# Kernel optimization log

Measured on AMD Instinct MI355X. Metric: run time of the kernel, lower is better.

The kernel has to match this reference:

```python
import jax, jax.numpy as jnp
import numpy as np

B = 256          # graphs per batch
NN = 400         # ROI nodes per graph (N*(N-1)/2 = 79800 = input_dim)
HID = [32, 64, 128]
KS = [200, 100, 50]   # nodes kept after each TopKPooling (ratio 0.5 each)
EPS = 1e-5


def setup_inputs() -> dict:
    key = jax.random.key(0)
    ks = jax.random.split(key, 20)
    # flattened strict upper triangle of a nonnegative FC matrix per sample
    data = jax.random.uniform(ks[0], (B, NN * (NN - 1) // 2), dtype=jnp.float32)
    inp = {"data": data}
    dims = [1] + HID
    for l in range(3):
        fan_in = dims[l]
        inp[f"W{l+1}"] = jax.random.normal(ks[1 + 5 * l], (dims[l], dims[l + 1]), jnp.float32) / np.sqrt(fan_in)
        inp[f"b{l+1}"] = jnp.zeros((dims[l + 1],), jnp.float32)
        inp[f"g{l+1}"] = jnp.ones((dims[l + 1],), jnp.float32)      # BN gamma
        inp[f"be{l+1}"] = jnp.zeros((dims[l + 1],), jnp.float32)    # BN beta
        inp[f"p{l+1}"] = jax.random.normal(ks[4 + 5 * l], (dims[l + 1],), jnp.float32) * 0.1  # TopK score vector
    return inp


def _gcn_conv(A, X, W, b):
    # GCNConv with edge weights: add self loops (weight 1), symmetric D^-1/2 A D^-1/2
    n = A.shape[1]
    Al = A + jnp.eye(n, dtype=A.dtype)[None]          # (B, n, n)
    deg = Al.sum(axis=-1)                             # (B, n)
    dis = jnp.where(deg > 0, jax.lax.rsqrt(deg), 0.0)
    An = dis[:, :, None] * Al * dis[:, None, :]
    return jnp.einsum('bij,bjf->bif', An, X @ W) + b


def _block(A, X, W, b, g, be, p, k):
    # GCNConv -> ReLU -> BatchNorm(train stats) -> (dropout=identity) -> TopKPooling
    h = jax.nn.relu(_gcn_conv(A, X, W, b))
    mu = h.mean(axis=(0, 1))
    var = h.var(axis=(0, 1))
    h = (h - mu) * jax.lax.rsqrt(var + EPS) * g + be
    # TopKPooling: score = x . p / ||p||, keep top k per graph, gate by tanh(score)
    score = h @ p / jnp.linalg.norm(p)                # (B, n)
    vals, idx = jax.lax.top_k(score, k)               # (B, k)
    Xn = jnp.take_along_axis(h, idx[:, :, None], axis=1) * jnp.tanh(vals)[:, :, None]
    bi = jnp.arange(A.shape[0])[:, None, None]
    An = A[bi, idx[:, :, None], idx[:, None, :]]      # filter_adj: edges among kept nodes
    return An, Xn


def reference(data, W1, b1, g1, be1, p1, W2, b2, g2, be2, p2, W3, b3, g3, be3, p3):
    Bn = data.shape[0]
    iu0, iu1 = np.triu_indices(NN, 1)
    A = jnp.zeros((Bn, NN, NN), data.dtype).at[:, iu0, iu1].set(data)
    A = A + jnp.swapaxes(A, 1, 2)                     # symmetric FC adjacency, zero diag
    X = jnp.ones((Bn, NN, 1), data.dtype)             # initial node feature dim = 1
    A, X = _block(A, X, W1, b1, g1, be1, p1, KS[0])
    A, X = _block(A, X, W2, b2, g2, be2, p2, KS[1])
    A, X = _block(A, X, W3, b3, g3, be3, p3, KS[2])
    return X.max(axis=1)                              # global_max_pool -> (B, 128)
```

## Files before the change

### kernel.cpp

```cpp
#include <hip/hip_runtime.h>
#include <math.h>

#define BB   256
#define NN0  400
#define NE   79800
#define EPSF 1e-5f

__device__ __forceinline__ int tri_e(int a, int c) {
  return a*(NN0-1) - ((a*(a-1))>>1) + (c - a - 1);
}

__device__ __forceinline__ size_t PRI(int b, int ti, int tj, int r) {
  return (((size_t)b*7 + ti)*7 + tj)*64 + r;
}

__device__ __forceinline__ float wave_sum(float v) {
  #pragma unroll
  for (int o = 32; o > 0; o >>= 1) v += __shfl_xor(v, o, 64);
  return v;
}

__device__ __forceinline__ void bitonic_desc(float* sc, int* si, int P) {
  const int tid = threadIdx.x;
  for (int k = 2; k <= P; k <<= 1) {
    for (int j = k >> 1; j > 0; j >>= 1) {
      __syncthreads();
      for (int i = tid; i < P; i += 256) {
        int ixj = i ^ j;
        if (ixj > i) {
          float a = sc[i], c = sc[ixj];
          int ai = si[i], ci = si[ixj];
          bool bef = (a > c) || (a == c && ai < ci);
          bool sw = ((i & k) == 0) ? !bef : bef;
          if (sw) { sc[i] = c; sc[ixj] = a; si[i] = ci; si[ixj] = ai; }
        }
      }
    }
  }
  __syncthreads();
}

__global__ __launch_bounds__(256) void k_tri_mv(
    const float* __restrict__ data,
    const float* __restrict__ pr_in, const float* __restrict__ pc_in,
    float* __restrict__ pr, float* __restrict__ pc) {
  __shared__ float tile[64][65];
  __shared__ float dI[64], dJ[64];
  const int q0 = blockIdx.x % 7, b = blockIdx.x / 7;
  const int tid = threadIdx.x;
  const int wave = tid >> 6, lane = tid & 63;
  const float* __restrict__ drow = data + (size_t)b*NE;
  int ti_a[4], tj_a[4];
  #pragma unroll
  for (int u = 0; u < 4; ++u) {
    int t = q0 + u*7;
    int ti = 0, rem = t;
    while (rem >= 7 - ti) { rem -= 7 - ti; ++ti; }
    ti_a[u] = ti; tj_a[u] = ti + rem;
  }
  float vreg[16];
  float rI = 0.f, rJ = 0.f;
  auto issue = [&](int u) {
    const int i0 = ti_a[u]*64, j0 = tj_a[u]*64;
    const int ni = min(64, NN0 - i0), nj = min(64, NN0 - j0);
    #pragma unroll
    for (int k = 0; k < 16; ++k) {
      const int rr = wave*16 + k;
      const int i = i0 + rr, j = j0 + lane;
      vreg[k] = 0.f;
      if (rr < ni && lane < nj && j > i) vreg[k] = drow[tri_e(i, j)];
    }
    if (pr_in) {
      if (tid < 64) {
        float a = 0.f;
        if (tid < ni) {
          const int tt = ti_a[u], r = tid;
          float acc = 1.f;
          for (int tj = tt; tj < 7; ++tj) acc += pr_in[PRI(b, tt, tj, r)];
          for (int ts = 0; ts <= tt; ++ts) acc += pc_in[PRI(b, ts, tt, r)];
          a = rsqrtf(acc);
        }
        rI = a;
      } else if (tid < 128) {
        const int c = tid - 64;
        float a = 0.f;
        if (c < nj) {
          const int tt = tj_a[u], r = c;
          float acc = 1.f;
          for (int tj = tt; tj < 7; ++tj) acc += pr_in[PRI(b, tt, tj, r)];
          for (int ts = 0; ts <= tt; ++ts) acc += pc_in[PRI(b, ts, tt, r)];
          a = rsqrtf(acc);
        }
        rJ = a;
      }
    } else {
      if (tid < 64) rI = (tid < ni) ? 1.f : 0.f;
      else if (tid < 128) rJ = (tid - 64 < nj) ? 1.f : 0.f;
    }
  };
  issue(0);
  #pragma unroll 1
  for (int u = 0; u < 4; ++u) {
    const int ti = ti_a[u], tj = tj_a[u];
    if (u) __syncthreads();
    #pragma unroll
    for (int k = 0; k < 16; ++k) tile[wave*16 + k][lane] = vreg[k];
    if (tid < 64) dI[tid] = rI;
    else if (tid < 128) dJ[tid-64] = rJ;
    __syncthreads();
    if (u + 1 < 4) issue(u + 1);
    {
      const int r = tid >> 2, q = tid & 3;
      float s = 0.f;
      #pragma unroll
      for (int c = 0; c < 16; ++c) s += tile[r][q*16 + c] * dJ[q*16 + c];
      s += __shfl_xor(s, 1, 64);
      s += __shfl_xor(s, 2, 64);
      if (q == 0) pr[PRI(b, ti, tj, r)] = s;
    }
    {
      const int c = tid >> 2, q = tid & 3;
      float s = 0.f;
      #pragma unroll
      for (int r = 0; r < 16; ++r) s += tile[q*16 + r][c] * dI[q*16 + r];
      s += __shfl_xor(s, 1, 64);
      s += __shfl_xor(s, 2, 64);
      if (q == 0) pc[PRI(b, ti, tj, c)] = s;
    }
  }
}

__global__ __launch_bounds__(256) void k_sfin_stats_red(
    const float* __restrict__ pr, const float* __restrict__ pc,
    const float* __restrict__ pr2, const float* __restrict__ pc2,
    const float* __restrict__ W1, const float* __restrict__ b1,
    float* __restrict__ s1, float* __restrict__ acc1) {
  __shared__ float sl[256];
  __shared__ float st[64];
  __shared__ float w1s[32], b1s[32];
  const int tid = threadIdx.x;
  const int i = blockIdx.x*256 + tid;
  if (tid < 32) { w1s[tid] = W1[tid]; b1s[tid] = b1[tid]; }
  if (tid < 64) st[tid] = 0.f;
  const int b = i / NN0, n = i % NN0;
  const int t = n >> 6, r = n & 63;
  float dacc = 1.f, sacc = 0.f;
  for (int tj = t; tj < 7; ++tj) { dacc += pr[PRI(b, t, tj, r)]; sacc += pr2[PRI(b, t, tj, r)]; }
  for (int ti = 0; ti <= t; ++ti) { dacc += pc[PRI(b, ti, t, r)]; sacc += pc2[PRI(b, ti, t, r)]; }
  const float d = rsqrtf(dacc);
  const float s = d * (d + sacc);
  s1[i] = s;
  sl[tid] = s;
  __syncthreads();
  const int f = tid & 31, sub = tid >> 5;
  const float w = w1s[f], bb = b1s[f];
  float S = 0.f, Q = 0.f;
  #pragma unroll
  for (int k = 0; k < 32; ++k) {
    const float ss = sl[sub*32 + k];
    const float h = fmaxf(ss*w + bb, 0.f);
    S += h; Q += h*h;
  }
  atomicAdd(&st[f], S);
  atomicAdd(&st[32+f], Q);
  __syncthreads();
  if (tid < 64) atomicAdd(&acc1[tid], st[tid]);
}

__global__ __launch_bounds__(256) void k_top1(
    const float* __restrict__ s1, const float* __restrict__ acc1,
    const float* __restrict__ W1, const float* __restrict__ b1,
    const float* __restrict__ g1, const float* __restrict__ be1,
    const float* __restrict__ p1, const float* __restrict__ W2,
    int* __restrict__ nodes2, int* __restrict__ sperm2, float* __restrict__ Y2) {
  __shared__ float sc[512]; __shared__ int si[512];
  __shared__ float sS[NN0];
  __shared__ float tvs[200];
  __shared__ int nds_l[200];
  __shared__ float w1s[32], b1s[32], cfs[32], scs[32], shs[32];
  __shared__ __align__(16) float hp[6400];
  __shared__ float c0s;
  const int tid = threadIdx.x, b = blockIdx.x;
  if (tid < 32) { w1s[tid] = W1[tid]; b1s[tid] = b1[tid]; }
  if (tid < 64) {
    float scale = 0.f, shift = 0.f, pv = 0.f;
    if (tid < 32) {
      const float S = acc1[tid], Q = acc1[32 + tid];
      const float N = 102400.f;
      const float mu = S / N;
      const float var = Q / N - mu*mu;
      const float inv = rsqrtf(var + EPSF);
      scale = inv * g1[tid];
      shift = be1[tid] - mu * scale;
      pv = p1[tid];
    }
    const float pn = sqrtf(wave_sum(pv*pv));
    if (tid < 32) { scs[tid] = scale; shs[tid] = shift; cfs[tid] = scale*pv/pn; }
    float u = (tid < 32) ? shift*pv/pn : 0.f;
    u = wave_sum(u);
    if (tid == 0) c0s = u;
  }
  __syncthreads();
  const float c0 = c0s;
  for (int i = tid; i < 512; i += 256) {
    if (i < NN0) {
      const float s = s1[(size_t)b*NN0 + i];
      sS[i] = s;
      float sco = c0;
      #pragma unroll
      for (int f = 0; f < 32; ++f) sco += fmaxf(s*w1s[f] + b1s[f], 0.f) * cfs[f];
      sc[i] = sco; si[i] = i;
    } else { sc[i] = -INFINITY; si[i] = 0x7fffffff; }
  }
  bitonic_desc(sc, si, 512);
  for (int k = tid; k < 200; k += 256) {
    tvs[k] = tanhf(sc[k]);
    nds_l[k] = si[k];
    nodes2[b*200 + k] = si[k];
  }
  __syncthreads();
  for (int o = tid; o < 6400; o += 256) {
    const int k = o >> 5, f = o & 31;
    const float s = sS[nds_l[k]];
    const float h = fmaxf(s*w1s[f] + b1s[f], 0.f);
    hp[o] = (h*scs[f] + shs[f]) * tvs[k];
  }
  __syncthreads();
  {
    const int g = tid & 63;
    float wr[32];
    #pragma unroll
    for (int f = 0; f < 32; ++f) wr[f] = W2[f*64 + g];
    for (int o = tid; o < 12800; o += 256) {
      const int k = o >> 6;
      float acc = 0.f;
      #pragma unroll
      for (int c4 = 0; c4 < 8; ++c4) {
        const float4 x4 = *(const float4*)&hp[(k<<5) + (c4<<2)];
        acc += x4.x*wr[c4*4] + x4.y*wr[c4*4+1] + x4.z*wr[c4*4+2] + x4.w*wr[c4*4+3];
      }
      Y2[(size_t)b*12800 + o] = acc;
    }
  }
  __syncthreads();
  if (tid < 256) {
    sc[tid] = (tid < 200) ? -(float)nds_l[tid] : -INFINITY;
    si[tid] = (tid < 200) ? tid : 0x7fffffff;
  }
  bitonic_desc(sc, si, 256);
  if (tid < 200) sperm2[b*200 + tid] = si[tid];
}

__global__ __launch_bounds__(256) void k_gatherA2(
    const float* __restrict__ data, const int* __restrict__ nodes2,
    const int* __restrict__ sperm2, float* __restrict__ A2, float* __restrict__ dis2) {
  __shared__ int nds[200], sp[200], sn[200];
  __shared__ float rowbuf[4][200];
  const int idx = blockIdx.x;
  const int r9 = idx >> 3;
  const int b = (idx & 7)*32 + r9/50;
  const int rg = r9 % 50;
  const int tid = threadIdx.x;
  if (tid < 200) { nds[tid] = nodes2[b*200 + tid]; sp[tid] = sperm2[b*200 + tid]; }
  __syncthreads();
  if (tid < 200) sn[tid] = nds[sp[tid]];
  __syncthreads();
  const int wave = tid >> 6, lane = tid & 63;
  const int i = rg*4 + wave;
  const int ni = nds[i];
  const float* __restrict__ drow = data + (size_t)b*NE;
  float accd = 0.f;
  for (int jj = lane; jj < 200; jj += 64) {
    const int sj = sn[jj];
    float v = 0.f;
    if (sj != ni) {
      const int a = min(ni, sj), c = max(ni, sj);
      v = drow[tri_e(a, c)];
    }
    rowbuf[wave][sp[jj]] = v;
    accd += v;
  }
  __syncthreads();
  for (int j = lane; j < 200; j += 64)
    A2[((size_t)b*200 + i)*200 + j] = rowbuf[wave][j];
  accd = wave_sum(accd);
  if (lane == 0) dis2[b*200 + i] = rsqrtf(1.f + accd);
}

__global__ __launch_bounds__(256) void k_conv2(
    const float* __restrict__ A2, const float* __restrict__ Y2,
    const float* __restrict__ dis2, const float* __restrict__ b2,
    float* __restrict__ h2g, float* __restrict__ acc2g) {
  __shared__ __align__(16) float ab[40*64];
  __shared__ __align__(16) float zb[40*64];
  __shared__ float st[128];
  const int tid = threadIdx.x;
  const int b = blockIdx.x >> 2, p = blockIdx.x & 3;
  const int tx = tid & 15, ty = tid >> 4;
  if (tid < 128) st[tid] = 0.f;
  const float4 bv = *(const float4*)&b2[tx<<2];
  float acc[4][4] = {};
  #pragma unroll 1
  for (int j0 = 0; j0 < 200; j0 += 40) {
    __syncthreads();
    for (int t = tid; t < 640; t += 256) {
      const int js = t >> 4, f4 = t & 15;
      const float dz = dis2[b*200 + j0 + js];
      float4 v = *(const float4*)&Y2[((size_t)b*200 + (j0 + js))*64 + (f4 << 2)];
      v.x *= dz; v.y *= dz; v.z *= dz; v.w *= dz;
      *(float4*)&zb[(js << 6) + (f4 << 2)] = v;
    }
    for (int t = tid; t < 640; t += 256) {
      const int js = t >> 4, c4l = t & 15;
      const int cg = (p << 6) + (c4l << 2);
      float4 v = make_float4(0.f, 0.f, 0.f, 0.f);
      if (cg < 200)
        v = *(const float4*)&A2[((size_t)b*200 + (j0 + js))*200 + cg];
      *(float4*)&ab[(js << 6) + (c4l << 2)] = v;
    }
    __syncthreads();
    #pragma unroll 2
    for (int js = 0; js < 40; ++js) {
      const float4 a4 = *(const float4*)&ab[(js << 6) + (ty << 2)];
      const float4 z4 = *(const float4*)&zb[(js << 6) + (tx << 2)];
      acc[0][0] += a4.x*z4.x; acc[0][1] += a4.x*z4.y; acc[0][2] += a4.x*z4.z; acc[0][3] += a4.x*z4.w;
      acc[1][0] += a4.y*z4.x; acc[1][1] += a4.y*z4.y; acc[1][2] += a4.y*z4.z; acc[1][3] += a4.y*z4.w;
      acc[2][0] += a4.z*z4.x; acc[2][1] += a4.z*z4.y; acc[2][2] += a4.z*z4.z; acc[2][3] += a4.z*z4.w;
      acc[3][0] += a4.w*z4.x; acc[3][1] += a4.w*z4.y; acc[3][2] += a4.w*z4.z; acc[3][3] += a4.w*z4.w;
    }
  }
  float ss[4] = {0,0,0,0}, qq[4] = {0,0,0,0};
  #pragma unroll
  for (int qr = 0; qr < 4; ++qr) {
    const int r = (p << 6) + (ty << 2) + qr;
    if (r < 200) {
      const float d = dis2[b*200 + r];
      const float dd = d*d;
      const float4 zi = *(const float4*)&Y2[((size_t)b*200 + r)*64 + (tx << 2)];
      const float h0 = fmaxf(d*acc[qr][0] + dd*zi.x + bv.x, 0.f);
      const float h1 = fmaxf(d*acc[qr][1] + dd*zi.y + bv.y, 0.f);
      const float h2v = fmaxf(d*acc[qr][2] + dd*zi.z + bv.z, 0.f);
      const float h3v = fmaxf(d*acc[qr][3] + dd*zi.w + bv.w, 0.f);
      *(float4*)&h2g[((size_t)b*200 + r)*64 + (tx<<2)] = make_float4(h0,h1,h2v,h3v);
      ss[0]+=h0; ss[1]+=h1; ss[2]+=h2v; ss[3]+=h3v;
      qq[0]+=h0*h0; qq[1]+=h1*h1; qq[2]+=h2v*h2v; qq[3]+=h3v*h3v;
    }
  }
  #pragma unroll
  for (int qf = 0; qf < 4; ++qf) {
    atomicAdd(&st[(tx<<2)+qf], ss[qf]);
    atomicAdd(&st[64+(tx<<2)+qf], qq[qf]);
  }
  __syncthreads();
  if (tid < 128) atomicAdd(&acc2g[tid], st[tid]);
}

__global__ __launch_bounds__(256) void k_top2(
    const float* __restrict__ h2g, const float* __restrict__ acc2,
    const float* __restrict__ g2, const float* __restrict__ be2,
    const float* __restrict__ p2, const float* __restrict__ W3,
    const int* __restrict__ nodes2, int* __restrict__ nodes3,
    float* __restrict__ Y3) {
  __shared__ float sc[256]; __shared__ int si[256];
  __shared__ __align__(16) float xs[6400];
  __shared__ float sc2[64], sh2[64], cf2[64];
  __shared__ float c20s;
  const int tid = threadIdx.x, b = blockIdx.x;
  if (tid < 64) {
    const float S = acc2[tid], Q = acc2[64 + tid];
    const float N = 51200.f;
    const float mu = S/N, var = Q/N - mu*mu, inv = rsqrtf(var + EPSF);
    const float scale = inv*g2[tid], shift = be2[tid] - mu*scale;
    const float pv = p2[tid];
    const float pn = sqrtf(wave_sum(pv*pv));
    sc2[tid] = scale; sh2[tid] = shift; cf2[tid] = scale*pv/pn;
    const float u = wave_sum(shift*pv/pn);
    if (tid == 0) c20s = u;
  }
  __syncthreads();
  const int wave = tid >> 6, lane = tid & 63;
  const float cf = cf2[lane];
  const float c20 = c20s;
  for (int i = wave; i < 200; i += 4) {
    float v = h2g[((size_t)b*200 + i)*64 + lane] * cf;
    v = wave_sum(v);
    if (lane == 0) { sc[i] = v + c20; si[i] = i; }
  }
  if (tid >= 200) { sc[tid] = -INFINITY; si[tid] = 0x7fffffff; }
  bitonic_desc(sc, si, 256);
  const float scale = sc2[lane], shift = sh2[lane];
  for (int o = tid; o < 6400; o += 256) {
    const int k = o >> 6;
    const int idx = si[k];
    const float tv = tanhf(sc[k]);
    xs[o] = (h2g[((size_t)b*200 + idx)*64 + lane] * scale + shift) * tv;
  }
  for (int k = tid; k < 100; k += 256) nodes3[b*100 + k] = nodes2[b*200 + si[k]];
  __syncthreads();
  {
    const int g = tid & 127;
    float wr[64];
    #pragma unroll
    for (int f = 0; f < 64; ++f) wr[f] = W3[f*128 + g];
    for (int o = tid; o < 12800; o += 256) {
      const int k = o >> 7;
      float acc = 0.f;
      #pragma unroll
      for (int c4 = 0; c4 < 16; ++c4) {
        const float4 x4 = *(const float4*)&xs[(k<<6) + (c4<<2)];
        acc += x4.x*wr[c4*4] + x4.y*wr[c4*4+1] + x4.z*wr[c4*4+2] + x4.w*wr[c4*4+3];
      }
      Y3[(size_t)b*12800 + o] = acc;
    }
  }
}

__global__ __launch_bounds__(256) void k_gatherA3(
    const float* __restrict__ data, const int* __restrict__ nodes3,
    float* __restrict__ A3, float* __restrict__ dis3) {
  __shared__ int nds[100];
  const int b = blockIdx.x / 25, rg = blockIdx.x % 25;
  const int tid = threadIdx.x;
  if (tid < 100) nds[tid] = nodes3[b*100 + tid];
  __syncthreads();
  const int wave = tid >> 6, lane = tid & 63;
  const int i = rg*4 + wave;
  const int ni = nds[i];
  const float* __restrict__ drow = data + (size_t)b*NE;
  float accd = 0.f;
  for (int j = lane; j < 100; j += 64) {
    float v = 0.f;
    if (j != i) {
      const int nj = nds[j];
      const int a = min(ni, nj), c = max(ni, nj);
      v = drow[tri_e(a, c)];
    }
    A3[((size_t)b*100 + i)*100 + j] = v;
    accd += v;
  }
  accd = wave_sum(accd);
  if (lane == 0) dis3[b*100 + i] = rsqrtf(1.f + accd);
}

__global__ __launch_bounds__(256) void k_conv3(
    const float* __restrict__ A3, const float* __restrict__ Y3,
    const float* __restrict__ dis3, const float* __restrict__ b3,
    float* __restrict__ h3g, float* __restrict__ acc3g) {
  __shared__ __align__(16) float z[100*128];
  __shared__ __align__(16) float ab[32*32];
  __shared__ float st[256];
  const int tid = threadIdx.x;
  const int b = blockIdx.x >> 2, p = blockIdx.x & 3;
  const int tx = tid & 31, ty = tid >> 5;
  for (int t = tid; t < 12800; t += 256)
    z[t] = Y3[(size_t)b*12800 + t] * dis3[b*100 + (t >> 7)];
  st[tid] = 0.f;
  const float4 bv = *(const float4*)&b3[tx<<2];
  float acc[4][4] = {};
  #pragma unroll 1
  for (int j0 = 0; j0 < 100; j0 += 32) {
    const int nj = (j0 + 32 <= 100) ? 32 : (100 - j0);
    __syncthreads();
    for (int t = tid; t < nj*32; t += 256) {
      const int js = t >> 5, lr = t & 31;
      const int c = (p << 5) + lr;
      ab[t] = (c < 100) ? A3[((size_t)b*100 + (j0 + js))*100 + c] : 0.f;
    }
    __syncthreads();
    for (int js = 0; js < nj; ++js) {
      const float4 a4 = *(const float4*)&ab[(js<<5) + (ty<<2)];
      const float4 z4 = *(const float4*)&z[((j0+js)<<7) + (tx<<2)];
      acc[0][0] += a4.x*z4.x; acc[0][1] += a4.x*z4.y; acc[0][2] += a4.x*z4.z; acc[0][3] += a4.x*z4.w;
      acc[1][0] += a4.y*z4.x; acc[1][1] += a4.y*z4.y; acc[1][2] += a4.y*z4.z; acc[1][3] += a4.y*z4.w;
      acc[2][0] += a4.z*z4.x; acc[2][1] += a4.z*z4.y; acc[2][2] += a4.z*z4.z; acc[2][3] += a4.z*z4.w;
      acc[3][0] += a4.w*z4.x; acc[3][1] += a4.w*z4.y; acc[3][2] += a4.w*z4.z; acc[3][3] += a4.w*z4.w;
    }
  }
  float ss[4] = {0,0,0,0}, qq[4] = {0,0,0,0};
  #pragma unroll
  for (int qr = 0; qr < 4; ++qr) {
    const int r = (p << 5) + (ty << 2) + qr;
    if (r < 100) {
      const float d = dis3[b*100 + r];
      const float4 zi = *(const float4*)&z[(r << 7) + (tx << 2)];
      const float h0 = fmaxf(d*(acc[qr][0] + zi.x) + bv.x, 0.f);
      const float h1 = fmaxf(d*(acc[qr][1] + zi.y) + bv.y, 0.f);
      const float h2v = fmaxf(d*(acc[qr][2] + zi.z) + bv.z, 0.f);
      const float h3v = fmaxf(d*(acc[qr][3] + zi.w) + bv.w, 0.f);
      *(float4*)&h3g[((size_t)b*100 + r)*128 + (tx<<2)] = make_float4(h0,h1,h2v,h3v);
      ss[0]+=h0; ss[1]+=h1; ss[2]+=h2v; ss[3]+=h3v;
      qq[0]+=h0*h0; qq[1]+=h1*h1; qq[2]+=h2v*h2v; qq[3]+=h3v*h3v;
    }
  }
  #pragma unroll
  for (int qf = 0; qf < 4; ++qf) {
    atomicAdd(&st[(tx<<2)+qf], ss[qf]);
    atomicAdd(&st[128+(tx<<2)+qf], qq[qf]);
  }
  __syncthreads();
  atomicAdd(&acc3g[tid], st[tid]);
}

__global__ __launch_bounds__(256) void k_top3(
    const float* __restrict__ h3g, const float* __restrict__ acc3,
    const float* __restrict__ g3, const float* __restrict__ be3,
    const float* __restrict__ p3, float* __restrict__ out) {
  __shared__ float sc[128]; __shared__ int si[128]; __shared__ float tv[64];
  __shared__ float scl[128], shl[128], cfl[128];
  __shared__ float red2[4];
  const int tid = threadIdx.x, b = blockIdx.x;
  const int wave = tid >> 6, lane = tid & 63;
  float scale = 0.f, shift = 0.f, pv = 0.f;
  if (tid < 128) {
    const float S = acc3[tid], Q = acc3[128 + tid];
    const float N = 25600.f;
    const float mu = S/N, var = Q/N - mu*mu, inv = rsqrtf(var + EPSF);
    scale = inv*g3[tid]; shift = be3[tid] - mu*scale; pv = p3[tid];
    const float t2 = wave_sum(pv*pv);
    if (lane == 0) red2[wave] = t2;
  }
  __syncthreads();
  const float pn = sqrtf(red2[0] + red2[1]);
  if (tid < 128) {
    scl[tid] = scale; shl[tid] = shift; cfl[tid] = scale*pv/pn;
    const float u = wave_sum(shift*pv/pn);
    if (lane == 0) red2[2 + wave] = u;
  }
  __syncthreads();
  const float c30 = red2[2] + red2[3];
  const float clo = cfl[lane], chi = cfl[64 + lane];
  for (int i = wave; i < 100; i += 4) {
    const float* hr = h3g + ((size_t)b*100 + i)*128;
    float v = hr[lane]*clo + hr[64 + lane]*chi;
    v = wave_sum(v);
    if (lane == 0) { sc[i] = v + c30; si[i] = i; }
  }
  if (tid >= 100 && tid < 128) { sc[tid] = -INFINITY; si[tid] = 0x7fffffff; }
  bitonic_desc(sc, si, 128);
  if (tid < 50) tv[tid] = tanhf(sc[tid]);
  __syncthreads();
  if (tid < 128) {
    const float scalev = scl[tid], shiftv = shl[tid];
    float m = -INFINITY;
    for (int k = 0; k < 50; ++k) {
      const float h = h3g[((size_t)b*100 + si[k])*128 + tid];
      m = fmaxf(m, (h*scalev + shiftv)*tv[k]);
    }
    out[(size_t)b*128 + tid] = m;
  }
}

extern "C" void kernel_launch(void* const* d_in, const int* in_sizes, int n_in,
                              void* d_out, int out_size, void* d_ws, size_t ws_size,
                              hipStream_t stream) {
  (void)in_sizes; (void)n_in; (void)out_size; (void)ws_size;
  const float* data = (const float*)d_in[0];
  const float* W1 = (const float*)d_in[1];
  const float* b1 = (const float*)d_in[2];
  const float* g1 = (const float*)d_in[3];
  const float* be1 = (const float*)d_in[4];
  const float* p1 = (const float*)d_in[5];
  const float* W2 = (const float*)d_in[6];
  const float* b2 = (const float*)d_in[7];
  const float* g2 = (const float*)d_in[8];
  const float* be2 = (const float*)d_in[9];
  const float* p2 = (const float*)d_in[10];
  const float* W3 = (const float*)d_in[11];
  const float* b3 = (const float*)d_in[12];
  const float* g3 = (const float*)d_in[13];
  const float* be3 = (const float*)d_in[14];
  const float* p3 = (const float*)d_in[15];
  float* out = (float*)d_out;

  char* ws = (char*)d_ws;
  size_t off = 0;
  auto alloc = [&](size_t n) { size_t o = off; off += (n + 255) & ~(size_t)255; return o; };
  float* pr     = (float*)(ws + alloc((size_t)BB*49*64*4));
  float* pc     = (float*)(ws + alloc((size_t)BB*49*64*4));
  float* pr2    = (float*)(ws + alloc((size_t)BB*49*64*4));
  float* pc2    = (float*)(ws + alloc((size_t)BB*49*64*4));
  float* s1     = (float*)(ws + alloc((size_t)BB*NN0*4));
  float* accz   = (float*)(ws + alloc(448*4));
  int*   nodes2 = (int*)  (ws + alloc((size_t)BB*200*4));
  int*   sperm2 = (int*)  (ws + alloc((size_t)BB*200*4));
  float* Y2     = (float*)(ws + alloc((size_t)BB*12800*4));
  float* A2     = (float*)(ws + alloc((size_t)BB*40000*4));
  float* dis2   = (float*)(ws + alloc((size_t)BB*200*4));
  float* h2     = (float*)(ws + alloc((size_t)BB*12800*4));
  int*   nodes3 = (int*)  (ws + alloc((size_t)BB*100*4));
  float* Y3     = (float*)(ws + alloc((size_t)BB*12800*4));
  float* A3     = (float*)(ws + alloc((size_t)BB*10000*4));
  float* dis3   = (float*)(ws + alloc((size_t)BB*100*4));
  float* h3     = (float*)(ws + alloc((size_t)BB*12800*4));
  float* acc1 = accz;
  float* acc2 = accz + 64;
  float* acc3 = accz + 192;

  hipMemsetAsync(accz, 0, 448*4, stream);
  k_tri_mv<<<dim3(BB*7), dim3(256), 0, stream>>>(data, nullptr, nullptr, pr, pc);
  k_tri_mv<<<dim3(BB*7), dim3(256), 0, stream>>>(data, pr, pc, pr2, pc2);
  k_sfin_stats_red<<<dim3(400), dim3(256), 0, stream>>>(pr, pc, pr2, pc2, W1, b1, s1, acc1);
  k_top1<<<dim3(BB), dim3(256), 0, stream>>>(s1, acc1, W1, b1, g1, be1, p1, W2, nodes2, sperm2, Y2);
  k_gatherA2<<<dim3(BB*50), dim3(256), 0, stream>>>(data, nodes2, sperm2, A2, dis2);
  k_conv2<<<dim3(BB*4), dim3(256), 0, stream>>>(A2, Y2, dis2, b2, h2, acc2);
  k_top2<<<dim3(BB), dim3(256), 0, stream>>>(h2, acc2, g2, be2, p2, W3, nodes2, nodes3, Y3);
  k_gatherA3<<<dim3(BB*25), dim3(256), 0, stream>>>(data, nodes3, A3, dis3);
  k_conv3<<<dim3(BB*4), dim3(256), 0, stream>>>(A3, Y3, dis3, b3, h3, acc3);
  k_top3<<<dim3(BB), dim3(256), 0, stream>>>(h3, acc3, g3, be3, p3, out);
}
```

Before: 466.1 us.

## Retile GCN conv kernels across more blocks and widen top-k kernels to 512 threads

Both graph-convolution kernels now split each graph's output rows over 7 blocks instead of 4. The mapping becomes one lane per feature with a few rows per wave. conv3 also stages its features in 25-row chunks instead of holding the whole 100x128 matrix in shared memory, which cuts LDS use and should raise occupancy. The top-k/projection kernels for layers 1 and 2 run with 512 threads, and the bitonic sort now strides by blockDim. The aim is more parallelism and better latency hiding, at the cost of more redundant feature loads per graph and more partial-stat atomics.

```diff
diff --git a/kernel.cpp b/kernel.cpp
--- a/kernel.cpp
+++ b/kernel.cpp
@@ -22,10 +22,11 @@
 
 __device__ __forceinline__ void bitonic_desc(float* sc, int* si, int P) {
   const int tid = threadIdx.x;
+  const int nt = blockDim.x;
   for (int k = 2; k <= P; k <<= 1) {
     for (int j = k >> 1; j > 0; j >>= 1) {
       __syncthreads();
-      for (int i = tid; i < P; i += 256) {
+      for (int i = tid; i < P; i += nt) {
         int ixj = i ^ j;
         if (ixj > i) {
           float a = sc[i], c = sc[ixj];
@@ -167,7 +168,7 @@
   if (tid < 64) atomicAdd(&acc1[tid], st[tid]);
 }
 
-__global__ __launch_bounds__(256) void k_top1(
+__global__ __launch_bounds__(512) void k_top1(
     const float* __restrict__ s1, const float* __restrict__ acc1,
     const float* __restrict__ W1, const float* __restrict__ b1,
     const float* __restrict__ g1, const float* __restrict__ be1,
@@ -202,7 +203,7 @@
   }
   __syncthreads();
   const float c0 = c0s;
-  for (int i = tid; i < 512; i += 256) {
+  for (int i = tid; i < 512; i += 512) {
     if (i < NN0) {
       const float s = s1[(size_t)b*NN0 + i];
       sS[i] = s;
@@ -213,13 +214,13 @@
     } else { sc[i] = -INFINITY; si[i] = 0x7fffffff; }
   }
   bitonic_desc(sc, si, 512);
-  for (int k = tid; k < 200; k += 256) {
+  for (int k = tid; k < 200; k += 512) {
     tvs[k] = tanhf(sc[k]);
     nds_l[k] = si[k];
     nodes2[b*200 + k] = si[k];
   }
   __syncthreads();
-  for (int o = tid; o < 6400; o += 256) {
+  for (int o = tid; o < 6400; o += 512) {
     const int k = o >> 5, f = o & 31;
     const float s = sS[nds_l[k]];
     const float h = fmaxf(s*w1s[f] + b1s[f], 0.f);
@@ -231,7 +232,7 @@
     float wr[32];
     #pragma unroll
     for (int f = 0; f < 32; ++f) wr[f] = W2[f*64 + g];
-    for (int o = tid; o < 12800; o += 256) {
+    for (int o = tid; o < 12800; o += 512) {
       const int k = o >> 6;
       float acc = 0.f;
       #pragma unroll
@@ -291,18 +292,20 @@
     const float* __restrict__ A2, const float* __restrict__ Y2,
     const float* __restrict__ dis2, const float* __restrict__ b2,
     float* __restrict__ h2g, float* __restrict__ acc2g) {
-  __shared__ __align__(16) float ab[40*64];
   __shared__ __align__(16) float zb[40*64];
+  __shared__ __align__(16) float ab[40*32];
   __shared__ float st[128];
   const int tid = threadIdx.x;
-  const int b = blockIdx.x >> 2, p = blockIdx.x & 3;
-  const int tx = tid & 15, ty = tid >> 4;
+  const int b = blockIdx.x / 7, p = blockIdx.x % 7;
+  const int wave = tid >> 6, lane = tid & 63;
+  const int r0 = p*32;
   if (tid < 128) st[tid] = 0.f;
-  const float4 bv = *(const float4*)&b2[tx<<2];
-  float acc[4][4] = {};
+  const float bl = b2[lane];
+  float acc[8] = {0,0,0,0,0,0,0,0};
   #pragma unroll 1
-  for (int j0 = 0; j0 < 200; j0 += 40) {
-    __syncthreads();
+  for (int s = 0; s < 5; ++s) {
+    const int j0 = s*40;
+    if (s) __syncthreads();
     for (int t = tid; t < 640; t += 256) {
       const int js = t >> 4, f4 = t & 15;
       const float dz = dis2[b*200 + j0 + js];
@@ -310,52 +313,43 @@
       v.x *= dz; v.y *= dz; v.z *= dz; v.w *= dz;
       *(float4*)&zb[(js << 6) + (f4 << 2)] = v;
     }
-    for (int t = tid; t < 640; t += 256) {
-      const int js = t >> 4, c4l = t & 15;
-      const int cg = (p << 6) + (c4l << 2);
+    for (int t = tid; t < 320; t += 256) {
+      const int js = t >> 3, c4 = t & 7;
+      const int col = r0 + (c4 << 2);
       float4 v = make_float4(0.f, 0.f, 0.f, 0.f);
-      if (cg < 200)
-        v = *(const float4*)&A2[((size_t)b*200 + (j0 + js))*200 + cg];
-      *(float4*)&ab[(js << 6) + (c4l << 2)] = v;
+      if (col <= 196)
+        v = *(const float4*)&A2[((size_t)b*200 + (j0 + js))*200 + col];
+      *(float4*)&ab[(js << 5) + (c4 << 2)] = v;
     }
     __syncthreads();
-    #pragma unroll 2
+    #pragma unroll 4
     for (int js = 0; js < 40; ++js) {
-      const float4 a4 = *(const float4*)&ab[(js << 6) + (ty << 2)];
-      const float4 z4 = *(const float4*)&zb[(js << 6) + (tx << 2)];
-      acc[0][0] += a4.x*z4.x; acc[0][1] += a4.x*z4.y; acc[0][2] += a4.x*z4.z; acc[0][3] += a4.x*z4.w;
-      acc[1][0] += a4.y*z4.x; acc[1][1] += a4.y*z4.y; acc[1][2] += a4.y*z4.z; acc[1][3] += a4.y*z4.w;
-      acc[2][0] += a4.z*z4.x; acc[2][1] += a4.z*z4.y; acc[2][2] += a4.z*z4.z; acc[2][3] += a4.z*z4.w;
-      acc[3][0] += a4.w*z4.x; acc[3][1] += a4.w*z4.y; acc[3][2] += a4.w*z4.z; acc[3][3] += a4.w*z4.w;
-    }
-  }
-  float ss[4] = {0,0,0,0}, qq[4] = {0,0,0,0};
+      const float z = zb[(js << 6) + lane];
+      const float4 a0 = *(const float4*)&ab[(js << 5) + (wave << 3)];
+      const float4 a1 = *(const float4*)&ab[(js << 5) + (wave << 3) + 4];
+      acc[0] += a0.x*z; acc[1] += a0.y*z; acc[2] += a0.z*z; acc[3] += a0.w*z;
+      acc[4] += a1.x*z; acc[5] += a1.y*z; acc[6] += a1.z*z; acc[7] += a1.w*z;
+    }
+  }
+  float ss = 0.f, qq = 0.f;
   #pragma unroll
-  for (int qr = 0; qr < 4; ++qr) {
-    const int r = (p << 6) + (ty << 2) + qr;
+  for (int k = 0; k < 8; ++k) {
+    const int r = r0 + (wave << 3) + k;
     if (r < 200) {
       const float d = dis2[b*200 + r];
-      const float dd = d*d;
-      const float4 zi = *(const float4*)&Y2[((size_t)b*200 + r)*64 + (tx << 2)];
-      const float h0 = fmaxf(d*acc[qr][0] + dd*zi.x + bv.x, 0.f);
-      const float h1 = fmaxf(d*acc[qr][1] + dd*zi.y + bv.y, 0.f);
-      const float h2v = fmaxf(d*acc[qr][2] + dd*zi.z + bv.z, 0.f);
-      const float h3v = fmaxf(d*acc[qr][3] + dd*zi.w + bv.w, 0.f);
-      *(float4*)&h2g[((size_t)b*200 + r)*64 + (tx<<2)] = make_float4(h0,h1,h2v,h3v);
-      ss[0]+=h0; ss[1]+=h1; ss[2]+=h2v; ss[3]+=h3v;
-      qq[0]+=h0*h0; qq[1]+=h1*h1; qq[2]+=h2v*h2v; qq[3]+=h3v*h3v;
-    }
-  }
-  #pragma unroll
-  for (int qf = 0; qf < 4; ++qf) {
-    atomicAdd(&st[(tx<<2)+qf], ss[qf]);
-    atomicAdd(&st[64+(tx<<2)+qf], qq[qf]);
-  }
+      const float y = Y2[((size_t)b*200 + r)*64 + lane];
+      const float h = fmaxf(d*acc[k] + d*d*y + bl, 0.f);
+      h2g[((size_t)b*200 + r)*64 + lane] = h;
+      ss += h; qq += h*h;
+    }
+  }
+  atomicAdd(&st[lane], ss);
+  atomicAdd(&st[64 + lane], qq);
   __syncthreads();
   if (tid < 128) atomicAdd(&acc2g[tid], st[tid]);
 }
 
-__global__ __launch_bounds__(256) void k_top2(
+__global__ __launch_bounds__(512) void k_top2(
     const float* __restrict__ h2g, const float* __restrict__ acc2,
     const float* __restrict__ g2, const float* __restrict__ be2,
     const float* __restrict__ p2, const float* __restrict__ W3,
@@ -381,28 +375,28 @@
   const int wave = tid >> 6, lane = tid & 63;
   const float cf = cf2[lane];
   const float c20 = c20s;
-  for (int i = wave; i < 200; i += 4) {
+  for (int i = wave; i < 200; i += 8) {
     float v = h2g[((size_t)b*200 + i)*64 + lane] * cf;
     v = wave_sum(v);
     if (lane == 0) { sc[i] = v + c20; si[i] = i; }
   }
-  if (tid >= 200) { sc[tid] = -INFINITY; si[tid] = 0x7fffffff; }
+  if (tid >= 200 && tid < 256) { sc[tid] = -INFINITY; si[tid] = 0x7fffffff; }
   bitonic_desc(sc, si, 256);
   const float scale = sc2[lane], shift = sh2[lane];
-  for (int o = tid; o < 6400; o += 256) {
+  for (int o = tid; o < 6400; o += 512) {
     const int k = o >> 6;
     const int idx = si[k];
     const float tv = tanhf(sc[k]);
     xs[o] = (h2g[((size_t)b*200 + idx)*64 + lane] * scale + shift) * tv;
   }
-  for (int k = tid; k < 100; k += 256) nodes3[b*100 + k] = nodes2[b*200 + si[k]];
+  for (int k = tid; k < 100; k += 512) nodes3[b*100 + k] = nodes2[b*200 + si[k]];
   __syncthreads();
   {
     const int g = tid & 127;
     float wr[64];
     #pragma unroll
     for (int f = 0; f < 64; ++f) wr[f] = W3[f*128 + g];
-    for (int o = tid; o < 12800; o += 256) {
+    for (int o = tid; o < 12800; o += 512) {
       const int k = o >> 7;
       float acc = 0.f;
       #pragma unroll
@@ -446,57 +440,64 @@
     const float* __restrict__ A3, const float* __restrict__ Y3,
     const float* __restrict__ dis3, const float* __restrict__ b3,
     float* __restrict__ h3g, float* __restrict__ acc3g) {
-  __shared__ __align__(16) float z[100*128];
-  __shared__ __align__(16) float ab[32*32];
+  __shared__ __align__(16) float zb[25*128];
+  __shared__ __align__(16) float ab[25*16];
   __shared__ float st[256];
   const int tid = threadIdx.x;
-  const int b = blockIdx.x >> 2, p = blockIdx.x & 3;
-  const int tx = tid & 31, ty = tid >> 5;
-  for (int t = tid; t < 12800; t += 256)
-    z[t] = Y3[(size_t)b*12800 + t] * dis3[b*100 + (t >> 7)];
+  const int b = blockIdx.x / 7, p = blockIdx.x % 7;
+  const int wave = tid >> 6, lane = tid & 63;
+  const int r0 = p*16;
   st[tid] = 0.f;
-  const float4 bv = *(const float4*)&b3[tx<<2];
-  float acc[4][4] = {};
+  const float bl0 = b3[lane], bl1 = b3[64 + lane];
+  float acc0[4] = {0,0,0,0}, acc1[4] = {0,0,0,0};
   #pragma unroll 1
-  for (int j0 = 0; j0 < 100; j0 += 32) {
-    const int nj = (j0 + 32 <= 100) ? 32 : (100 - j0);
+  for (int s = 0; s < 4; ++s) {
+    const int j0 = s*25;
+    if (s) __syncthreads();
+    for (int t = tid; t < 800; t += 256) {
+      const int js = t >> 5, f4 = t & 31;
+      const float dz = dis3[b*100 + j0 + js];
+      float4 v = *(const float4*)&Y3[((size_t)b*100 + (j0 + js))*128 + (f4 << 2)];
+      v.x *= dz; v.y *= dz; v.z *= dz; v.w *= dz;
+      *(float4*)&zb[(js << 7) + (f4 << 2)] = v;
+    }
+    for (int t = tid; t < 100; t += 256) {
+      const int js = t >> 2, c4 = t & 3;
+      const int col = r0 + (c4 << 2);
+      float4 v = make_float4(0.f, 0.f, 0.f, 0.f);
+      if (col <= 96)
+        v = *(const float4*)&A3[((size_t)b*100 + (j0 + js))*100 + col];
+      *(float4*)&ab[(js << 4) + (c4 << 2)] = v;
+    }
     __syncthreads();
-    for (int t = tid; t < nj*32; t += 256) {
-      const int js = t >> 5, lr = t & 31;
-      const int c = (p << 5) + lr;
-      ab[t] = (c < 100) ? A3[((size_t)b*100 + (j0 + js))*100 + c] : 0.f;
-    }
-    __syncthreads();
-    for (int js = 0; js < nj; ++js) {
-      const float4 a4 = *(const float4*)&ab[(js<<5) + (ty<<2)];
-      const float4 z4 = *(const float4*)&z[((j0+js)<<7) + (tx<<2)];
-      acc[0][0] += a4.x*z4.x; acc[0][1] += a4.x*z4.y; acc[0][2] += a4.x*z4.z; acc[0][3] += a4.x*z4.w;
-      acc[1][0] += a4.y*z4.x; acc[1][1] += a4.y*z4.y; acc[1][2] += a4.y*z4.z; acc[1][3] += a4.y*z4.w;
-      acc[2][0] += a4.z*z4.x; acc[2][1] += a4.z*z4.y; acc[2][2] += a4.z*z4.z; acc[2][3] += a4.z*z4.w;
-      acc[3][0] += a4.w*z4.x; acc[3][1] += a4.w*z4.y; acc[3][2] += a4.w*z4.z; acc[3][3] += a4.w*z4.w;
-    }
-  }
-  float ss[4] = {0,0,0,0}, qq[4] = {0,0,0,0};
+    #pragma unroll 5
+    for (int js = 0; js < 25; ++js) {
+      const float z0 = zb[(js << 7) + lane];
+      const float z1 = zb[(js << 7) + 64 + lane];
+      const float4 a4 = *(const float4*)&ab[(js << 4) + (wave << 2)];
+      acc0[0] += a4.x*z0; acc0[1] += a4.y*z0; acc0[2] += a4.z*z0; acc0[3] += a4.w*z0;
+      acc1[0] += a4.x*z1; acc1[1] += a4.y*z1; acc1[2] += a4.z*z1; acc1[3] += a4.w*z1;
+    }
+  }
+  float ss0 = 0.f, qq0 = 0.f, ss1 = 0.f, qq1 = 0.f;
   #pragma unroll
-  for (int qr = 0; qr < 4; ++qr) {
-    const int r = (p << 5) + (ty << 2) + qr;
+  for (int k = 0; k < 4; ++k) {
+    const int r = r0 + (wave << 2) + k;
     if (r < 100) {
       const float d = dis3[b*100 + r];
-      const float4 zi = *(const float4*)&z[(r << 7) + (tx << 2)];
-      const float h0 = fmaxf(d*(acc[qr][0] + zi.x) + bv.x, 0.f);
-      const float h1 = fmaxf(d*(acc[qr][1] + zi.y) + bv.y, 0.f);
-      const float h2v = fmaxf(d*(acc[qr][2] + zi.z) + bv.z, 0.f);
-      const float h3v = fmaxf(d*(acc[qr][3] + zi.w) + bv.w, 0.f);
-      *(float4*)&h3g[((size_t)b*100 + r)*128 + (tx<<2)] = make_float4(h0,h1,h2v,h3v);
-      ss[0]+=h0; ss[1]+=h1; ss[2]+=h2v; ss[3]+=h3v;
-      qq[0]+=h0*h0; qq[1]+=h1*h1; qq[2]+=h2v*h2v; qq[3]+=h3v*h3v;
-    }
-  }
-  #pragma unroll
-  for (int qf = 0; qf < 4; ++qf) {
-    atomicAdd(&st[(tx<<2)+qf], ss[qf]);
-    atomicAdd(&st[128+(tx<<2)+qf], qq[qf]);
-  }
+      const float y0 = Y3[((size_t)b*100 + r)*128 + lane];
+      const float y1 = Y3[((size_t)b*100 + r)*128 + 64 + lane];
+      const float h0 = fmaxf(d*acc0[k] + d*d*y0 + bl0, 0.f);
+      const float h1 = fmaxf(d*acc1[k] + d*d*y1 + bl1, 0.f);
+      h3g[((size_t)b*100 + r)*128 + lane] = h0;
+      h3g[((size_t)b*100 + r)*128 + 64 + lane] = h1;
+      ss0 += h0; qq0 += h0*h0; ss1 += h1; qq1 += h1*h1;
+    }
+  }
+  atomicAdd(&st[lane], ss0);
+  atomicAdd(&st[64 + lane], ss1);
+  atomicAdd(&st[128 + lane], qq0);
+  atomicAdd(&st[192 + lane], qq1);
   __syncthreads();
   atomicAdd(&acc3g[tid], st[tid]);
 }
@@ -600,11 +601,11 @@
   k_tri_mv<<<dim3(BB*7), dim3(256), 0, stream>>>(data, nullptr, nullptr, pr, pc);
   k_tri_mv<<<dim3(BB*7), dim3(256), 0, stream>>>(data, pr, pc, pr2, pc2);
   k_sfin_stats_red<<<dim3(400), dim3(256), 0, stream>>>(pr, pc, pr2, pc2, W1, b1, s1, acc1);
-  k_top1<<<dim3(BB), dim3(256), 0, stream>>>(s1, acc1, W1, b1, g1, be1, p1, W2, nodes2, sperm2, Y2);
+  k_top1<<<dim3(BB), dim3(512), 0, stream>>>(s1, acc1, W1, b1, g1, be1, p1, W2, nodes2, sperm2, Y2);
   k_gatherA2<<<dim3(BB*50), dim3(256), 0, stream>>>(data, nodes2, sperm2, A2, dis2);
-  k_conv2<<<dim3(BB*4), dim3(256), 0, stream>>>(A2, Y2, dis2, b2, h2, acc2);
-  k_top2<<<dim3(BB), dim3(256), 0, stream>>>(h2, acc2, g2, be2, p2, W3, nodes2, nodes3, Y3);
+  k_conv2<<<dim3(BB*7), dim3(256), 0, stream>>>(A2, Y2, dis2, b2, h2, acc2);
+  k_top2<<<dim3(BB), dim3(512), 0, stream>>>(h2, acc2, g2, be2, p2, W3, nodes2, nodes3, Y3);
   k_gatherA3<<<dim3(BB*25), dim3(256), 0, stream>>>(data, nodes3, A3, dis3);
-  k_conv3<<<dim3(BB*4), dim3(256), 0, stream>>>(A3, Y3, dis3, b3, h3, acc3);
+  k_conv3<<<dim3(BB*7), dim3(256), 0, stream>>>(A3, Y3, dis3, b3, h3, acc3);
   k_top3<<<dim3(BB), dim3(256), 0, stream>>>(h3, acc3, g3, be3, p3, out);
 }
```

After: 482.8 us. +3.6%, slower.
